# Performance work log

Hardware: AMD Instinct MI355X
Metric: run time of the kernel (lower is better)

Reference implementation:

```python
import jax, jax.numpy as jnp
import numpy as np

N_NODES = 50000
N_EDGES = 800000
D_IN = 128
D_HID = 128
D_OUT = 128
EPS = 0.1  # GINConv eps


def setup_inputs() -> dict:
    key = jax.random.key(0)
    k = jax.random.split(key, 8)
    scale = 1.0 / np.sqrt(D_IN)
    return {
        "x": jax.random.normal(k[0], (N_NODES, D_IN), dtype=jnp.float32),
        "edge_index": jax.random.randint(k[1], (2, N_EDGES), 0, N_NODES, dtype=jnp.int64),
        "edge_weight": jax.random.uniform(k[2], (N_EDGES,), dtype=jnp.float32),
        "W1a": jax.random.normal(k[3], (D_IN, D_HID), dtype=jnp.float32) * scale,
        "W1b": jax.random.normal(k[4], (D_HID, D_HID), dtype=jnpp.float32) if False else jax.random.normal(k[4], (D_HID, D_HID), dtype=jnp.float32) * scale,
        "W2a": jax.random.normal(k[5], (D_HID, D_HID), dtype=jnp.float32) * scale,
        "W2b": jax.random.normal(k[6], (D_HID, D_OUT), dtype=jnp.float32) * scale,
    }


def _gin_conv(h, src, dst, ew, Wa, Wb, n_nodes):
    # edge-weighted neighbor sum: aggr[i] = sum_{(j->i)} w_ji * h[j]
    msg = ew[:, None] * h[src]                       # [E, d]
    aggr = jax.ops.segment_sum(msg, dst, num_segments=n_nodes)  # [N, d]
    z = (1.0 + EPS) * h + aggr                       # GIN update
    # 2-layer bias-free MLP: lin -> relu -> lin
    return jnp.maximum(z @ Wa, 0.0) @ Wb


def reference(x, edge_index, edge_weight, W1a, W1b, W2a, W2b):
    src, dst = edge_index[0], edge_index[1]
    n = x.shape[0]
    h = _gin_conv(x, src, dst, edge_weight, W1a, W1b, n)
    h = jnp.maximum(h, 0.0)  # relu between convs; dropout is identity in eval
    h = _gin_conv(h, src, dst, edge_weight, W2a, W2b, n)
    return h
```

## Files before the change

kernel.cpp:

```cpp
#include <hip/hip_runtime.h>
#include <hip/hip_fp16.h>

#define D 128
#define N_NODES 50000
#define EPSP1 1.1f

#define NPB 256
#define NBUCK 196
#define CAP 5120
#define P1E 2048
#define TS 136

typedef __attribute__((ext_vector_type(8))) short short8;
typedef __attribute__((ext_vector_type(4))) float f32x4;

__device__ __forceinline__ unsigned short f2bf(float f) {
    unsigned u = __float_as_uint(f);
    u += 0x7FFF + ((u >> 16) & 1);
    return (unsigned short)(u >> 16);
}
__device__ __forceinline__ float bf2f(unsigned short h) {
    return __uint_as_float(((unsigned)h) << 16);
}

__global__ __launch_bounds__(256) void pass1_bucket(
    const int* __restrict__ src, const int* __restrict__ dst,
    const float* __restrict__ ew, int* __restrict__ gcnt,
    uint2* __restrict__ gstage, int ne)
{
    __shared__ int bcnt[NBUCK];
    __shared__ int goff[NBUCK];
    int tid = threadIdx.x;
    int bid = blockIdx.x;
    if (tid < NBUCK) bcnt[tid] = 0;
    __syncthreads();
    int e0 = bid * P1E;
    int   rank[8];
    int   buck[8];
    uint2 pay[8];
#pragma unroll
    for (int j = 0; j < 8; ++j) {
        int e = e0 + j * 256 + tid;
        buck[j] = -1;
        if (e < ne) {
            int d_ = dst[e];
            int b  = d_ >> 8;
            int dl = d_ & 255;
            pay[j].x = (unsigned)(src[e] & 0xFFFF) | ((unsigned)dl << 16);
            pay[j].y = (unsigned)__half_as_ushort(__float2half_rn(ew[e]));
            rank[j]  = atomicAdd(&bcnt[b], 1);
            buck[j]  = b;
        }
    }
    __syncthreads();
    if (tid < NBUCK && bcnt[tid] > 0)
        goff[tid] = atomicAdd(&gcnt[tid], bcnt[tid]);
    __syncthreads();
#pragma unroll
    for (int j = 0; j < 8; ++j) {
        if (buck[j] >= 0) {
            int pos = goff[buck[j]] + rank[j];
            if (pos < CAP)
                gstage[(size_t)buck[j] * CAP + pos] = pay[j];
        }
    }
}

__global__ __launch_bounds__(512) void fused_mid(
    const uint2* __restrict__ gstage, const int* __restrict__ gcnt,
    unsigned* __restrict__ epay, int* __restrict__ off,
    const float* __restrict__ x, unsigned short* __restrict__ hb, int n4,
    const float* __restrict__ W1a, const float* __restrict__ W1b,
    const float* __restrict__ W2a, const float* __restrict__ W2b,
    unsigned short* __restrict__ wp)
{
    __shared__ int hist[NPB];
    __shared__ int scn[NPB];
    __shared__ int loc[NPB];
    __shared__ int wtot[8];
    __shared__ int base_s;
    __shared__ unsigned csr[CAP];

    int bid = blockIdx.x;
    int t = threadIdx.x;

    if (bid < NBUCK) {
        int b = bid;
        int cnt = min(gcnt[b], CAP);

        if (t < NPB) hist[t] = 0;
        __syncthreads();

        uint2 ent[CAP / 512];
#pragma unroll
        for (int it = 0; it < CAP / 512; ++it) {
            int i = it * 512 + t;
            if (i < cnt) {
                ent[it] = gstage[(size_t)b * CAP + i];
                atomicAdd(&hist[(ent[it].x >> 16) & 255], 1);
            }
        }
        __syncthreads();

        int w = t >> 6, l = t & 63;
        if (w < 4) {
            int v = hist[w * 64 + l];
#pragma unroll
            for (int dd = 1; dd < 64; dd <<= 1) {
                int u = __shfl_up(v, dd, 64);
                if (l >= dd) v += u;
            }
            scn[w * 64 + l] = v;
            if (l == 63) wtot[w] = v;
        } else if (w == 4) {
            int v = 0;
            for (int i = l; i < NBUCK; i += 64)
                if (i < b) v += min(gcnt[i], CAP);
#pragma unroll
            for (int dd = 32; dd > 0; dd >>= 1) v += __shfl_down(v, dd, 64);
            if (l == 0) base_s = v;
        }
        __syncthreads();

        if (t < NPB) {
            int pre = 0;
#pragma unroll
            for (int j = 0; j < 3; ++j) if (j < w) pre += wtot[j];
            int incl = scn[t] + pre;
            int excl = incl - hist[t];
            int node = (b << 8) + t;
            if (node <= N_NODES) off[node] = base_s + excl;
            loc[t] = excl;
        }
        __syncthreads();

#pragma unroll
        for (int it = 0; it < CAP / 512; ++it) {
            int i = it * 512 + t;
            if (i < cnt) {
                int dl = (ent[it].x >> 16) & 255;
                int p = atomicAdd(&loc[dl], 1);
                csr[p] = (ent[it].x & 0xFFFF) | (ent[it].y << 16);
            }
        }
        __syncthreads();

        for (int i = t; i < cnt; i += 512)
            epay[base_s + i] = csr[i];
    } else if (bid < NBUCK + 782) {
        int base = (bid - NBUCK) * 2048;
#pragma unroll
        for (int it = 0; it < 4; ++it) {
            int i = base + it * 512 + t;
            if (i < n4) {
                float4 v = ((const float4*)x)[i];
                ushort4 o;
                o.x = f2bf(v.x); o.y = f2bf(v.y); o.z = f2bf(v.z); o.w = f2bf(v.w);
                ((ushort4*)hb)[i] = o;
            }
        }
    } else {
        int e2 = (bid - NBUCK - 782) * 512 + t;
        int mat = e2 >> 11;
        int e   = e2 & 2047;
        const float* W = (mat == 0) ? W1a : (mat == 1) ? W1b : (mat == 2) ? W2a : W2b;
        unsigned short* Wp = wp + (size_t)mat * 16384;
        int col = e & 127;
        int kq  = e >> 7;
        short8 v;
#pragma unroll
        for (int j = 0; j < 8; ++j)
            v[j] = (short)f2bf(W[(size_t)(kq * 8 + j) * 128 + col]);
        ((short8*)Wp)[e] = v;
    }
}

__global__ __launch_bounds__(256) void gather_kernel(
    const unsigned short* __restrict__ h, const int* __restrict__ off,
    const unsigned* __restrict__ epay, unsigned short* __restrict__ z, int n_nodes)
{
    int tid = threadIdx.x;
    int node = blockIdx.x * 4 + (tid >> 6);
    if (node >= n_nodes) return;
    int lane = tid & 63;
    int qtr  = lane >> 4;
    int sub  = lane & 15;
    int beg = off[node];
    int end = off[node + 1];
    float acc[8];
#pragma unroll
    for (int c = 0; c < 8; ++c) acc[c] = 0.f;

    int i = beg;
    for (; i + 16 <= end; i += 16) {
        unsigned p0 = epay[i + qtr];
        unsigned p1 = epay[i + 4 + qtr];
        unsigned p2 = epay[i + 8 + qtr];
        unsigned p3 = epay[i + 12 + qtr];
        short8 v0 = ((const short8*)(h + (size_t)(p0 & 0xFFFF) * D))[sub];
        short8 v1 = ((const short8*)(h + (size_t)(p1 & 0xFFFF) * D))[sub];
        short8 v2 = ((const short8*)(h + (size_t)(p2 & 0xFFFF) * D))[sub];
        short8 v3 = ((const short8*)(h + (size_t)(p3 & 0xFFFF) * D))[sub];
        float w0 = __half2float(__ushort_as_half((unsigned short)(p0 >> 16)));
        float w1 = __half2float(__ushort_as_half((unsigned short)(p1 >> 16)));
        float w2 = __half2float(__ushort_as_half((unsigned short)(p2 >> 16)));
        float w3 = __half2float(__ushort_as_half((unsigned short)(p3 >> 16)));
#pragma unroll
        for (int c = 0; c < 8; ++c)
            acc[c] += w0 * bf2f((unsigned short)v0[c]) + w1 * bf2f((unsigned short)v1[c])
                    + w2 * bf2f((unsigned short)v2[c]) + w3 * bf2f((unsigned short)v3[c]);
    }
    for (; i + 8 <= end; i += 8) {
        unsigned p0 = epay[i + qtr];
        unsigned p1 = epay[i + 4 + qtr];
        short8 v0 = ((const short8*)(h + (size_t)(p0 & 0xFFFF) * D))[sub];
        short8 v1 = ((const short8*)(h + (size_t)(p1 & 0xFFFF) * D))[sub];
        float w0 = __half2float(__ushort_as_half((unsigned short)(p0 >> 16)));
        float w1 = __half2float(__ushort_as_half((unsigned short)(p1 >> 16)));
#pragma unroll
        for (int c = 0; c < 8; ++c)
            acc[c] += w0 * bf2f((unsigned short)v0[c]) + w1 * bf2f((unsigned short)v1[c]);
    }
    for (; i + qtr < end; i += 4) {
        unsigned p0 = epay[i + qtr];
        short8 v0 = ((const short8*)(h + (size_t)(p0 & 0xFFFF) * D))[sub];
        float w0 = __half2float(__ushort_as_half((unsigned short)(p0 >> 16)));
#pragma unroll
        for (int c = 0; c < 8; ++c)
            acc[c] += w0 * bf2f((unsigned short)v0[c]);
    }

#pragma unroll
    for (int c = 0; c < 8; ++c) {
        acc[c] += __shfl(acc[c], (lane + 32) & 63, 64);
        acc[c] += __shfl(acc[c], (lane + 16) & 63, 64);
    }

    if (qtr == 0) {
        short8 xv = ((const short8*)(h + (size_t)node * D))[sub];
        short8 o;
#pragma unroll
        for (int c = 0; c < 8; ++c) {
            float v = acc[c] + EPSP1 * bf2f((unsigned short)xv[c]);
            o[c] = (short)f2bf(v);
        }
        ((short8*)(z + (size_t)node * D))[sub] = o;
    }
}

template<int RELU2, int OUT_F32>
__global__ __launch_bounds__(256) void mlp_fused(
    const unsigned short* __restrict__ A,
    const unsigned short* __restrict__ WpA,
    const unsigned short* __restrict__ WpB,
    void* __restrict__ outv, int n)
{
    __shared__ unsigned short t[128 * TS];

    int tid  = threadIdx.x;
    int wave = tid >> 6;
    int lane = tid & 63;
    int quad = lane >> 4;
    int lc   = lane & 15;
    int rbase = blockIdx.x * 128 + wave * 32;
    int rloc  = wave * 32;

    const short8 zero8 = {0, 0, 0, 0, 0, 0, 0, 0};

    short8 a[2][4];
#pragma unroll
    for (int s = 0; s < 2; ++s) {
        int row = rbase + s * 16 + lc;
        const unsigned short* ap = A + (size_t)row * D;
#pragma unroll
        for (int kk = 0; kk < 4; ++kk)
            a[s][kk] = (row < n) ? *(const short8*)(ap + kk * 32 + quad * 8) : zero8;
    }

    f32x4 acc[2][8];
#pragma unroll
    for (int s = 0; s < 2; ++s)
#pragma unroll
        for (int c = 0; c < 8; ++c)
            acc[s][c] = (f32x4){0.f, 0.f, 0.f, 0.f};

#pragma unroll
    for (int cf = 0; cf < 8; ++cf) {
        short8 b[4];
#pragma unroll
        for (int kk = 0; kk < 4; ++kk)
            b[kk] = *(const short8*)(WpA + ((size_t)(kk * 4 + quad) * 128 + cf * 16 + lc) * 8);
#pragma unroll
        for (int kk = 0; kk < 4; ++kk) {
            acc[0][cf] = __builtin_amdgcn_mfma_f32_16x16x32_bf16(a[0][kk], b[kk], acc[0][cf], 0, 0, 0);
            acc[1][cf] = __builtin_amdgcn_mfma_f32_16x16x32_bf16(a[1][kk], b[kk], acc[1][cf], 0, 0, 0);
        }
    }

#pragma unroll
    for (int s = 0; s < 2; ++s)
#pragma unroll
        for (int reg = 0; reg < 4; ++reg) {
            int row = rloc + s * 16 + quad * 4 + reg;
#pragma unroll
            for (int cf = 0; cf < 8; ++cf)
                t[row * TS + cf * 16 + lc] = f2bf(fmaxf(acc[s][cf][reg], 0.f));
        }
    __syncthreads();

#pragma unroll
    for (int s = 0; s < 2; ++s) {
        int row = rloc + s * 16 + lc;
#pragma unroll
        for (int kk = 0; kk < 4; ++kk)
            a[s][kk] = *(const short8*)&t[row * TS + kk * 32 + quad * 8];
    }
#pragma unroll
    for (int s = 0; s < 2; ++s)
#pragma unroll
        for (int c = 0; c < 8; ++c)
            acc[s][c] = (f32x4){0.f, 0.f, 0.f, 0.f};

#pragma unroll
    for (int cf = 0; cf < 8; ++cf) {
        short8 b[4];
#pragma unroll
        for (int kk = 0; kk < 4; ++kk)
            b[kk] = *(const short8*)(WpB + ((size_t)(kk * 4 + quad) * 128 + cf * 16 + lc) * 8);
#pragma unroll
        for (int kk = 0; kk < 4; ++kk) {
            acc[0][cf] = __builtin_amdgcn_mfma_f32_16x16x32_bf16(a[0][kk], b[kk], acc[0][cf], 0, 0, 0);
            acc[1][cf] = __builtin_amdgcn_mfma_f32_16x16x32_bf16(a[1][kk], b[kk], acc[1][cf], 0, 0, 0);
        }
    }

#pragma unroll
    for (int s = 0; s < 2; ++s)
#pragma unroll
        for (int reg = 0; reg < 4; ++reg) {
            int row = rbase + s * 16 + quad * 4 + reg;
            if (row < n) {
#pragma unroll
                for (int cf = 0; cf < 8; ++cf) {
                    float v = acc[s][cf][reg];
                    if (RELU2) v = fmaxf(v, 0.f);
                    int col = cf * 16 + lc;
                    if (OUT_F32)
                        ((float*)outv)[(size_t)row * D + col] = v;
                    else
                        ((unsigned short*)outv)[(size_t)row * D + col] = f2bf(v);
                }
            }
        }
}

extern "C" void kernel_launch(void* const* d_in, const int* in_sizes, int n_in,
                              void* d_out, int out_size, void* d_ws, size_t ws_size,
                              hipStream_t stream) {
    const float* x   = (const float*)d_in[0];
    const int*   ei  = (const int*)d_in[1];
    const float* ew  = (const float*)d_in[2];
    const float* W1a = (const float*)d_in[3];
    const float* W1b = (const float*)d_in[4];
    const float* W2a = (const float*)d_in[5];
    const float* W2b = (const float*)d_in[6];
    float* out = (float*)d_out;

    int n_edges = in_sizes[2];
    const int* src = ei;
    const int* dst = ei + n_edges;

    size_t node_elems = (size_t)N_NODES * D;
    unsigned short* hb = (unsigned short*)d_ws;
    unsigned short* zb = hb + node_elems;
    unsigned short* wp = zb + node_elems;
    unsigned* epay = (unsigned*)(wp + 4 * 16384);
    uint2*  gstage = (uint2*)(epay + n_edges);
    int*    gcnt   = (int*)(gstage + (size_t)NBUCK * CAP);
    int*    off    = gcnt + NBUCK;

    int p1grid = (n_edges + P1E - 1) / P1E;
    int ggrid  = (N_NODES + 127) / 128;
    int agrid  = (N_NODES + 3) / 4;
    int n4     = (int)(node_elems / 4);

    hipMemsetAsync(gcnt, 0, NBUCK * sizeof(int), stream);

    pass1_bucket<<<p1grid, 256, 0, stream>>>(src, dst, ew, gcnt, gstage, n_edges);

    fused_mid<<<NBUCK + 782 + 16, 512, 0, stream>>>(
        gstage, gcnt, epay, off,
        x, hb, n4, W1a, W1b, W2a, W2b, wp);

    unsigned short* wp0 = wp;
    unsigned short* wp1 = wp + 16384;
    unsigned short* wp2 = wp + 2 * 16384;
    unsigned short* wp3 = wp + 3 * 16384;

    gather_kernel<<<agrid, 256, 0, stream>>>(hb, off, epay, zb, N_NODES);
    mlp_fused<1, 0><<<ggrid, 256, 0, stream>>>(zb, wp0, wp1, hb, N_NODES);

    gather_kernel<<<agrid, 256, 0, stream>>>(hb, off, epay, zb, N_NODES);
    mlp_fused<0, 1><<<ggrid, 256, 0, stream>>>(zb, wp2, wp3, out, N_NODES);
}
```

Measured before the change: 202.8 us.

## Fuse neighbor gather with MLP per conv and move conversions into bucketing pass

The gather kernel and the two-layer MLP kernel are merged into one conv kernel. Each wave aggregates 16 nodes into shared memory, then runs both MFMA matmuls on them, so the intermediate z tensor never goes through global memory. Conv 1 now writes its output to zb and conv 2 reads from zb, which avoids overwriting hb while other blocks still gather from it. The x-to-bf16 and weight-packing work moves from the CSR build kernel into the edge-bucketing kernel, and the CSR build kernel keeps only bucket processing. The trade-off is that gathers are serialized per wave over 16 nodes, which can lower memory-level parallelism, and the MLP now runs on 16-row tiles per wave, so weights are reused less.

New measurement: 277.7 us. 36.9% more time.

```diff
diff --git a/kernel.cpp b/kernel.cpp
--- a/kernel.cpp
+++ b/kernel.cpp
@@ -23,56 +23,87 @@
     return __uint_as_float(((unsigned)h) << 16);
 }
 
-__global__ __launch_bounds__(256) void pass1_bucket(
+__global__ __launch_bounds__(256) void pass1_all(
     const int* __restrict__ src, const int* __restrict__ dst,
     const float* __restrict__ ew, int* __restrict__ gcnt,
-    uint2* __restrict__ gstage, int ne)
+    uint2* __restrict__ gstage, int ne, int nb1,
+    const float* __restrict__ x, unsigned short* __restrict__ hb,
+    int n4, int ncvt,
+    const float* __restrict__ W1a, const float* __restrict__ W1b,
+    const float* __restrict__ W2a, const float* __restrict__ W2b,
+    unsigned short* __restrict__ wp)
 {
     __shared__ int bcnt[NBUCK];
     __shared__ int goff[NBUCK];
     int tid = threadIdx.x;
     int bid = blockIdx.x;
-    if (tid < NBUCK) bcnt[tid] = 0;
-    __syncthreads();
-    int e0 = bid * P1E;
-    int   rank[8];
-    int   buck[8];
-    uint2 pay[8];
-#pragma unroll
-    for (int j = 0; j < 8; ++j) {
-        int e = e0 + j * 256 + tid;
-        buck[j] = -1;
-        if (e < ne) {
-            int d_ = dst[e];
-            int b  = d_ >> 8;
-            int dl = d_ & 255;
-            pay[j].x = (unsigned)(src[e] & 0xFFFF) | ((unsigned)dl << 16);
-            pay[j].y = (unsigned)__half_as_ushort(__float2half_rn(ew[e]));
-            rank[j]  = atomicAdd(&bcnt[b], 1);
-            buck[j]  = b;
-        }
-    }
-    __syncthreads();
-    if (tid < NBUCK && bcnt[tid] > 0)
-        goff[tid] = atomicAdd(&gcnt[tid], bcnt[tid]);
-    __syncthreads();
-#pragma unroll
-    for (int j = 0; j < 8; ++j) {
-        if (buck[j] >= 0) {
-            int pos = goff[buck[j]] + rank[j];
-            if (pos < CAP)
-                gstage[(size_t)buck[j] * CAP + pos] = pay[j];
-        }
-    }
-}
-
-__global__ __launch_bounds__(512) void fused_mid(
+
+    if (bid < nb1) {
+        if (tid < NBUCK) bcnt[tid] = 0;
+        __syncthreads();
+        int e0 = bid * P1E;
+        int   rank[8];
+        int   buck[8];
+        uint2 pay[8];
+#pragma unroll
+        for (int j = 0; j < 8; ++j) {
+            int e = e0 + j * 256 + tid;
+            buck[j] = -1;
+            if (e < ne) {
+                int d_ = dst[e];
+                int b  = d_ >> 8;
+                int dl = d_ & 255;
+                pay[j].x = (unsigned)(src[e] & 0xFFFF) | ((unsigned)dl << 16);
+                pay[j].y = (unsigned)__half_as_ushort(__float2half_rn(ew[e]));
+                rank[j]  = atomicAdd(&bcnt[b], 1);
+                buck[j]  = b;
+            }
+        }
+        __syncthreads();
+        if (tid < NBUCK && bcnt[tid] > 0)
+            goff[tid] = atomicAdd(&gcnt[tid], bcnt[tid]);
+        __syncthreads();
+#pragma unroll
+        for (int j = 0; j < 8; ++j) {
+            if (buck[j] >= 0) {
+                int pos = goff[buck[j]] + rank[j];
+                if (pos < CAP)
+                    gstage[(size_t)buck[j] * CAP + pos] = pay[j];
+            }
+        }
+    } else if (bid < nb1 + ncvt) {
+        int base = (bid - nb1) * 2048;
+#pragma unroll
+        for (int it = 0; it < 8; ++it) {
+            int i = base + it * 256 + tid;
+            if (i < n4) {
+                float4 v = ((const float4*)x)[i];
+                ushort4 o;
+                o.x = f2bf(v.x); o.y = f2bf(v.y); o.z = f2bf(v.z); o.w = f2bf(v.w);
+                ((ushort4*)hb)[i] = o;
+            }
+        }
+    } else {
+        int e2 = (bid - nb1 - ncvt) * 256 + tid;
+        if (e2 < 8192) {
+            int mat = e2 >> 11;
+            int e   = e2 & 2047;
+            const float* W = (mat == 0) ? W1a : (mat == 1) ? W1b : (mat == 2) ? W2a : W2b;
+            unsigned short* Wp = wp + (size_t)mat * 16384;
+            int col = e & 127;
+            int kq  = e >> 7;
+            short8 v;
+#pragma unroll
+            for (int j = 0; j < 8; ++j)
+                v[j] = (short)f2bf(W[(size_t)(kq * 8 + j) * 128 + col]);
+            ((short8*)Wp)[e] = v;
+        }
+    }
+}
+
+__global__ __launch_bounds__(512) void csr_build(
     const uint2* __restrict__ gstage, const int* __restrict__ gcnt,
-    unsigned* __restrict__ epay, int* __restrict__ off,
-    const float* __restrict__ x, unsigned short* __restrict__ hb, int n4,
-    const float* __restrict__ W1a, const float* __restrict__ W1b,
-    const float* __restrict__ W2a, const float* __restrict__ W2b,
-    unsigned short* __restrict__ wp)
+    unsigned* __restrict__ epay, int* __restrict__ off)
 {
     __shared__ int hist[NPB];
     __shared__ int scn[NPB];
@@ -81,277 +112,226 @@
     __shared__ int base_s;
     __shared__ unsigned csr[CAP];
 
-    int bid = blockIdx.x;
+    int b = blockIdx.x;
     int t = threadIdx.x;
-
-    if (bid < NBUCK) {
-        int b = bid;
-        int cnt = min(gcnt[b], CAP);
-
-        if (t < NPB) hist[t] = 0;
-        __syncthreads();
-
-        uint2 ent[CAP / 512];
-#pragma unroll
-        for (int it = 0; it < CAP / 512; ++it) {
-            int i = it * 512 + t;
-            if (i < cnt) {
-                ent[it] = gstage[(size_t)b * CAP + i];
-                atomicAdd(&hist[(ent[it].x >> 16) & 255], 1);
-            }
-        }
-        __syncthreads();
-
-        int w = t >> 6, l = t & 63;
-        if (w < 4) {
-            int v = hist[w * 64 + l];
-#pragma unroll
-            for (int dd = 1; dd < 64; dd <<= 1) {
-                int u = __shfl_up(v, dd, 64);
-                if (l >= dd) v += u;
-            }
-            scn[w * 64 + l] = v;
-            if (l == 63) wtot[w] = v;
-        } else if (w == 4) {
-            int v = 0;
-            for (int i = l; i < NBUCK; i += 64)
-                if (i < b) v += min(gcnt[i], CAP);
-#pragma unroll
-            for (int dd = 32; dd > 0; dd >>= 1) v += __shfl_down(v, dd, 64);
-            if (l == 0) base_s = v;
-        }
-        __syncthreads();
-
-        if (t < NPB) {
-            int pre = 0;
-#pragma unroll
-            for (int j = 0; j < 3; ++j) if (j < w) pre += wtot[j];
-            int incl = scn[t] + pre;
-            int excl = incl - hist[t];
-            int node = (b << 8) + t;
-            if (node <= N_NODES) off[node] = base_s + excl;
-            loc[t] = excl;
-        }
-        __syncthreads();
-
-#pragma unroll
-        for (int it = 0; it < CAP / 512; ++it) {
-            int i = it * 512 + t;
-            if (i < cnt) {
-                int dl = (ent[it].x >> 16) & 255;
-                int p = atomicAdd(&loc[dl], 1);
-                csr[p] = (ent[it].x & 0xFFFF) | (ent[it].y << 16);
-            }
-        }
-        __syncthreads();
-
-        for (int i = t; i < cnt; i += 512)
-            epay[base_s + i] = csr[i];
-    } else if (bid < NBUCK + 782) {
-        int base = (bid - NBUCK) * 2048;
-#pragma unroll
-        for (int it = 0; it < 4; ++it) {
-            int i = base + it * 512 + t;
-            if (i < n4) {
-                float4 v = ((const float4*)x)[i];
-                ushort4 o;
-                o.x = f2bf(v.x); o.y = f2bf(v.y); o.z = f2bf(v.z); o.w = f2bf(v.w);
-                ((ushort4*)hb)[i] = o;
-            }
-        }
-    } else {
-        int e2 = (bid - NBUCK - 782) * 512 + t;
-        int mat = e2 >> 11;
-        int e   = e2 & 2047;
-        const float* W = (mat == 0) ? W1a : (mat == 1) ? W1b : (mat == 2) ? W2a : W2b;
-        unsigned short* Wp = wp + (size_t)mat * 16384;
-        int col = e & 127;
-        int kq  = e >> 7;
-        short8 v;
-#pragma unroll
-        for (int j = 0; j < 8; ++j)
-            v[j] = (short)f2bf(W[(size_t)(kq * 8 + j) * 128 + col]);
-        ((short8*)Wp)[e] = v;
-    }
-}
-
-__global__ __launch_bounds__(256) void gather_kernel(
+    int cnt = min(gcnt[b], CAP);
+
+    if (t < NPB) hist[t] = 0;
+    __syncthreads();
+
+    uint2 ent[CAP / 512];
+#pragma unroll
+    for (int it = 0; it < CAP / 512; ++it) {
+        int i = it * 512 + t;
+        if (i < cnt) {
+            ent[it] = gstage[(size_t)b * CAP + i];
+            atomicAdd(&hist[(ent[it].x >> 16) & 255], 1);
+        }
+    }
+    __syncthreads();
+
+    int w = t >> 6, l = t & 63;
+    if (w < 4) {
+        int v = hist[w * 64 + l];
+#pragma unroll
+        for (int dd = 1; dd < 64; dd <<= 1) {
+            int u = __shfl_up(v, dd, 64);
+            if (l >= dd) v += u;
+        }
+        scn[w * 64 + l] = v;
+        if (l == 63) wtot[w] = v;
+    } else if (w == 4) {
+        int v = 0;
+        for (int i = l; i < NBUCK; i += 64)
+            if (i < b) v += min(gcnt[i], CAP);
+#pragma unroll
+        for (int dd = 32; dd > 0; dd >>= 1) v += __shfl_down(v, dd, 64);
+        if (l == 0) base_s = v;
+    }
+    __syncthreads();
+
+    if (t < NPB) {
+        int pre = 0;
+#pragma unroll
+        for (int j = 0; j < 3; ++j) if (j < w) pre += wtot[j];
+        int incl = scn[t] + pre;
+        int excl = incl - hist[t];
+        int node = (b << 8) + t;
+        if (node <= N_NODES) off[node] = base_s + excl;
+        loc[t] = excl;
+    }
+    __syncthreads();
+
+#pragma unroll
+    for (int it = 0; it < CAP / 512; ++it) {
+        int i = it * 512 + t;
+        if (i < cnt) {
+            int dl = (ent[it].x >> 16) & 255;
+            int p = atomicAdd(&loc[dl], 1);
+            csr[p] = (ent[it].x & 0xFFFF) | (ent[it].y << 16);
+        }
+    }
+    __syncthreads();
+
+    for (int i = t; i < cnt; i += 512)
+        epay[base_s + i] = csr[i];
+}
+
+template<int RELU2, int OUT_F32>
+__global__ __launch_bounds__(256) void conv_fused(
     const unsigned short* __restrict__ h, const int* __restrict__ off,
-    const unsigned* __restrict__ epay, unsigned short* __restrict__ z, int n_nodes)
-{
-    int tid = threadIdx.x;
-    int node = blockIdx.x * 4 + (tid >> 6);
-    if (node >= n_nodes) return;
-    int lane = tid & 63;
-    int qtr  = lane >> 4;
-    int sub  = lane & 15;
-    int beg = off[node];
-    int end = off[node + 1];
-    float acc[8];
-#pragma unroll
-    for (int c = 0; c < 8; ++c) acc[c] = 0.f;
-
-    int i = beg;
-    for (; i + 16 <= end; i += 16) {
-        unsigned p0 = epay[i + qtr];
-        unsigned p1 = epay[i + 4 + qtr];
-        unsigned p2 = epay[i + 8 + qtr];
-        unsigned p3 = epay[i + 12 + qtr];
-        short8 v0 = ((const short8*)(h + (size_t)(p0 & 0xFFFF) * D))[sub];
-        short8 v1 = ((const short8*)(h + (size_t)(p1 & 0xFFFF) * D))[sub];
-        short8 v2 = ((const short8*)(h + (size_t)(p2 & 0xFFFF) * D))[sub];
-        short8 v3 = ((const short8*)(h + (size_t)(p3 & 0xFFFF) * D))[sub];
-        float w0 = __half2float(__ushort_as_half((unsigned short)(p0 >> 16)));
-        float w1 = __half2float(__ushort_as_half((unsigned short)(p1 >> 16)));
-        float w2 = __half2float(__ushort_as_half((unsigned short)(p2 >> 16)));
-        float w3 = __half2float(__ushort_as_half((unsigned short)(p3 >> 16)));
-#pragma unroll
-        for (int c = 0; c < 8; ++c)
-            acc[c] += w0 * bf2f((unsigned short)v0[c]) + w1 * bf2f((unsigned short)v1[c])
-                    + w2 * bf2f((unsigned short)v2[c]) + w3 * bf2f((unsigned short)v3[c]);
-    }
-    for (; i + 8 <= end; i += 8) {
-        unsigned p0 = epay[i + qtr];
-        unsigned p1 = epay[i + 4 + qtr];
-        short8 v0 = ((const short8*)(h + (size_t)(p0 & 0xFFFF) * D))[sub];
-        short8 v1 = ((const short8*)(h + (size_t)(p1 & 0xFFFF) * D))[sub];
-        float w0 = __half2float(__ushort_as_half((unsigned short)(p0 >> 16)));
-        float w1 = __half2float(__ushort_as_half((unsigned short)(p1 >> 16)));
-#pragma unroll
-        for (int c = 0; c < 8; ++c)
-            acc[c] += w0 * bf2f((unsigned short)v0[c]) + w1 * bf2f((unsigned short)v1[c]);
-    }
-    for (; i + qtr < end; i += 4) {
-        unsigned p0 = epay[i + qtr];
-        short8 v0 = ((const short8*)(h + (size_t)(p0 & 0xFFFF) * D))[sub];
-        float w0 = __half2float(__ushort_as_half((unsigned short)(p0 >> 16)));
-#pragma unroll
-        for (int c = 0; c < 8; ++c)
-            acc[c] += w0 * bf2f((unsigned short)v0[c]);
-    }
-
-#pragma unroll
-    for (int c = 0; c < 8; ++c) {
-        acc[c] += __shfl(acc[c], (lane + 32) & 63, 64);
-        acc[c] += __shfl(acc[c], (lane + 16) & 63, 64);
-    }
-
-    if (qtr == 0) {
-        short8 xv = ((const short8*)(h + (size_t)node * D))[sub];
-        short8 o;
-#pragma unroll
-        for (int c = 0; c < 8; ++c) {
-            float v = acc[c] + EPSP1 * bf2f((unsigned short)xv[c]);
-            o[c] = (short)f2bf(v);
-        }
-        ((short8*)(z + (size_t)node * D))[sub] = o;
-    }
-}
-
-template<int RELU2, int OUT_F32>
-__global__ __launch_bounds__(256) void mlp_fused(
-    const unsigned short* __restrict__ A,
+    const unsigned* __restrict__ epay,
     const unsigned short* __restrict__ WpA,
     const unsigned short* __restrict__ WpB,
     void* __restrict__ outv, int n)
 {
-    __shared__ unsigned short t[128 * TS];
+    __shared__ unsigned short t[64 * TS];
 
     int tid  = threadIdx.x;
     int wave = tid >> 6;
     int lane = tid & 63;
-    int quad = lane >> 4;
-    int lc   = lane & 15;
-    int rbase = blockIdx.x * 128 + wave * 32;
-    int rloc  = wave * 32;
+    int qtr  = lane >> 4;
+    int sub  = lane & 15;
+    int rloc  = wave * 16;
+    int rbase = blockIdx.x * 64 + rloc;
 
     const short8 zero8 = {0, 0, 0, 0, 0, 0, 0, 0};
 
-    short8 a[2][4];
-#pragma unroll
-    for (int s = 0; s < 2; ++s) {
-        int row = rbase + s * 16 + lc;
-        const unsigned short* ap = A + (size_t)row * D;
-#pragma unroll
-        for (int kk = 0; kk < 4; ++kk)
-            a[s][kk] = (row < n) ? *(const short8*)(ap + kk * 32 + quad * 8) : zero8;
-    }
-
-    f32x4 acc[2][8];
-#pragma unroll
-    for (int s = 0; s < 2; ++s)
-#pragma unroll
-        for (int c = 0; c < 8; ++c)
-            acc[s][c] = (f32x4){0.f, 0.f, 0.f, 0.f};
+    for (int nd = 0; nd < 16; ++nd) {
+        int node = rbase + nd;
+        float acc[8];
+#pragma unroll
+        for (int c = 0; c < 8; ++c) acc[c] = 0.f;
+
+        if (node < n) {
+            int beg = off[node];
+            int end = off[node + 1];
+            int i = beg;
+            for (; i + 16 <= end; i += 16) {
+                unsigned p0 = epay[i + qtr];
+                unsigned p1 = epay[i + 4 + qtr];
+                unsigned p2 = epay[i + 8 + qtr];
+                unsigned p3 = epay[i + 12 + qtr];
+                short8 v0 = ((const short8*)(h + (size_t)(p0 & 0xFFFF) * D))[sub];
+                short8 v1 = ((const short8*)(h + (size_t)(p1 & 0xFFFF) * D))[sub];
+                short8 v2 = ((const short8*)(h + (size_t)(p2 & 0xFFFF) * D))[sub];
+                short8 v3 = ((const short8*)(h + (size_t)(p3 & 0xFFFF) * D))[sub];
+                float w0 = __half2float(__ushort_as_half((unsigned short)(p0 >> 16)));
+                float w1 = __half2float(__ushort_as_half((unsigned short)(p1 >> 16)));
+                float w2 = __half2float(__ushort_as_half((unsigned short)(p2 >> 16)));
+                float w3 = __half2float(__ushort_as_half((unsigned short)(p3 >> 16)));
+#pragma unroll
+                for (int c = 0; c < 8; ++c)
+                    acc[c] += w0 * bf2f((unsigned short)v0[c]) + w1 * bf2f((unsigned short)v1[c])
+                            + w2 * bf2f((unsigned short)v2[c]) + w3 * bf2f((unsigned short)v3[c]);
+            }
+            for (; i + 8 <= end; i += 8) {
+                unsigned p0 = epay[i + qtr];
+                unsigned p1 = epay[i + 4 + qtr];
+                short8 v0 = ((const short8*)(h + (size_t)(p0 & 0xFFFF) * D))[sub];
+                short8 v1 = ((const short8*)(h + (size_t)(p1 & 0xFFFF) * D))[sub];
+                float w0 = __half2float(__ushort_as_half((unsigned short)(p0 >> 16)));
+                float w1 = __half2float(__ushort_as_half((unsigned short)(p1 >> 16)));
+#pragma unroll
+                for (int c = 0; c < 8; ++c)
+                    acc[c] += w0 * bf2f((unsigned short)v0[c]) + w1 * bf2f((unsigned short)v1[c]);
+            }
+            for (; i + qtr < end; i += 4) {
+                unsigned p0 = epay[i + qtr];
+                short8 v0 = ((const short8*)(h + (size_t)(p0 & 0xFFFF) * D))[sub];
+                float w0 = __half2float(__ushort_as_half((unsigned short)(p0 >> 16)));
+#pragma unroll
+                for (int c = 0; c < 8; ++c)
+                    acc[c] += w0 * bf2f((unsigned short)v0[c]);
+            }
+        }
+
+#pragma unroll
+        for (int c = 0; c < 8; ++c) {
+            acc[c] += __shfl(acc[c], (lane + 32) & 63, 64);
+            acc[c] += __shfl(acc[c], (lane + 16) & 63, 64);
+        }
+
+        if (qtr == 0) {
+            short8 o;
+            if (node < n) {
+                short8 xv = ((const short8*)(h + (size_t)node * D))[sub];
+#pragma unroll
+                for (int c = 0; c < 8; ++c)
+                    o[c] = (short)f2bf(acc[c] + EPSP1 * bf2f((unsigned short)xv[c]));
+            } else {
+                o = zero8;
+            }
+            *(short8*)&t[(rloc + nd) * TS + sub * 8] = o;
+        }
+    }
+
+    short8 a[4];
+    {
+        int row = rloc + sub;
+#pragma unroll
+        for (int kk = 0; kk < 4; ++kk)
+            a[kk] = *(const short8*)&t[row * TS + kk * 32 + qtr * 8];
+    }
+    f32x4 acc2[8];
+#pragma unroll
+    for (int c = 0; c < 8; ++c) acc2[c] = (f32x4){0.f, 0.f, 0.f, 0.f};
 
 #pragma unroll
     for (int cf = 0; cf < 8; ++cf) {
         short8 b[4];
 #pragma unroll
         for (int kk = 0; kk < 4; ++kk)
-            b[kk] = *(const short8*)(WpA + ((size_t)(kk * 4 + quad) * 128 + cf * 16 + lc) * 8);
-#pragma unroll
-        for (int kk = 0; kk < 4; ++kk) {
-            acc[0][cf] = __builtin_amdgcn_mfma_f32_16x16x32_bf16(a[0][kk], b[kk], acc[0][cf], 0, 0, 0);
-            acc[1][cf] = __builtin_amdgcn_mfma_f32_16x16x32_bf16(a[1][kk], b[kk], acc[1][cf], 0, 0, 0);
-        }
-    }
-
-#pragma unroll
-    for (int s = 0; s < 2; ++s)
-#pragma unroll
-        for (int reg = 0; reg < 4; ++reg) {
-            int row = rloc + s * 16 + quad * 4 + reg;
-#pragma unroll
-            for (int cf = 0; cf < 8; ++cf)
-                t[row * TS + cf * 16 + lc] = f2bf(fmaxf(acc[s][cf][reg], 0.f));
-        }
-    __syncthreads();
-
-#pragma unroll
-    for (int s = 0; s < 2; ++s) {
-        int row = rloc + s * 16 + lc;
-#pragma unroll
-        for (int kk = 0; kk < 4; ++kk)
-            a[s][kk] = *(const short8*)&t[row * TS + kk * 32 + quad * 8];
-    }
-#pragma unroll
-    for (int s = 0; s < 2; ++s)
-#pragma unroll
-        for (int c = 0; c < 8; ++c)
-            acc[s][c] = (f32x4){0.f, 0.f, 0.f, 0.f};
+            b[kk] = *(const short8*)(WpA + ((size_t)(kk * 4 + qtr) * 128 + cf * 16 + sub) * 8);
+#pragma unroll
+        for (int kk = 0; kk < 4; ++kk)
+            acc2[cf] = __builtin_amdgcn_mfma_f32_16x16x32_bf16(a[kk], b[kk], acc2[cf], 0, 0, 0);
+    }
+
+#pragma unroll
+    for (int reg = 0; reg < 4; ++reg) {
+        int row = rloc + qtr * 4 + reg;
+#pragma unroll
+        for (int cf = 0; cf < 8; ++cf)
+            t[row * TS + cf * 16 + sub] = f2bf(fmaxf(acc2[cf][reg], 0.f));
+    }
+
+    {
+        int row = rloc + sub;
+#pragma unroll
+        for (int kk = 0; kk < 4; ++kk)
+            a[kk] = *(const short8*)&t[row * TS + kk * 32 + qtr * 8];
+    }
+#pragma unroll
+    for (int c = 0; c < 8; ++c) acc2[c] = (f32x4){0.f, 0.f, 0.f, 0.f};
 
 #pragma unroll
     for (int cf = 0; cf < 8; ++cf) {
         short8 b[4];
 #pragma unroll
         for (int kk = 0; kk < 4; ++kk)
-            b[kk] = *(const short8*)(WpB + ((size_t)(kk * 4 + quad) * 128 + cf * 16 + lc) * 8);
-#pragma unroll
-        for (int kk = 0; kk < 4; ++kk) {
-            acc[0][cf] = __builtin_amdgcn_mfma_f32_16x16x32_bf16(a[0][kk], b[kk], acc[0][cf], 0, 0, 0);
-            acc[1][cf] = __builtin_amdgcn_mfma_f32_16x16x32_bf16(a[1][kk], b[kk], acc[1][cf], 0, 0, 0);
-        }
-    }
-
-#pragma unroll
-    for (int s = 0; s < 2; ++s)
-#pragma unroll
-        for (int reg = 0; reg < 4; ++reg) {
-            int row = rbase + s * 16 + quad * 4 + reg;
-            if (row < n) {
-#pragma unroll
-                for (int cf = 0; cf < 8; ++cf) {
-                    float v = acc[s][cf][reg];
-                    if (RELU2) v = fmaxf(v, 0.f);
-                    int col = cf * 16 + lc;
-                    if (OUT_F32)
-                        ((float*)outv)[(size_t)row * D + col] = v;
-                    else
-                        ((unsigned short*)outv)[(size_t)row * D + col] = f2bf(v);
-                }
-            }
-        }
+            b[kk] = *(const short8*)(WpB + ((size_t)(kk * 4 + qtr) * 128 + cf * 16 + sub) * 8);
+#pragma unroll
+        for (int kk = 0; kk < 4; ++kk)
+            acc2[cf] = __builtin_amdgcn_mfma_f32_16x16x32_bf16(a[kk], b[kk], acc2[cf], 0, 0, 0);
+    }
+
+#pragma unroll
+    for (int reg = 0; reg < 4; ++reg) {
+        int row = rbase + qtr * 4 + reg;
+        if (row < n) {
+#pragma unroll
+            for (int cf = 0; cf < 8; ++cf) {
+                float v = acc2[cf][reg];
+                if (RELU2) v = fmaxf(v, 0.f);
+                int col = cf * 16 + sub;
+                if (OUT_F32)
+                    ((float*)outv)[(size_t)row * D + col] = v;
+                else
+                    ((unsigned short*)outv)[(size_t)row * D + col] = f2bf(v);
+            }
+        }
+    }
 }
 
 extern "C" void kernel_launch(void* const* d_in, const int* in_sizes, int n_in,
@@ -379,27 +359,26 @@
     int*    gcnt   = (int*)(gstage + (size_t)NBUCK * CAP);
     int*    off    = gcnt + NBUCK;
 
-    int p1grid = (n_edges + P1E - 1) / P1E;
-    int ggrid  = (N_NODES + 127) / 128;
-    int agrid  = (N_NODES + 3) / 4;
-    int n4     = (int)(node_elems / 4);
+    int nb1   = (n_edges + P1E - 1) / P1E;
+    int n4    = (int)(node_elems / 4);
+    int ncvt  = (n4 + 2047) / 2048;
+    int npack = 32;
+    int cgrid = (N_NODES + 63) / 64;
 
     hipMemsetAsync(gcnt, 0, NBUCK * sizeof(int), stream);
 
-    pass1_bucket<<<p1grid, 256, 0, stream>>>(src, dst, ew, gcnt, gstage, n_edges);
-
-    fused_mid<<<NBUCK + 782 + 16, 512, 0, stream>>>(
-        gstage, gcnt, epay, off,
-        x, hb, n4, W1a, W1b, W2a, W2b, wp);
+    pass1_all<<<nb1 + ncvt + npack, 256, 0, stream>>>(
+        src, dst, ew, gcnt, gstage, n_edges, nb1,
+        x, hb, n4, ncvt, W1a, W1b, W2a, W2b, wp);
+
+    csr_build<<<NBUCK, 512, 0, stream>>>(gstage, gcnt, epay, off);
 
     unsigned short* wp0 = wp;
     unsigned short* wp1 = wp + 16384;
     unsigned short* wp2 = wp + 2 * 16384;
     unsigned short* wp3 = wp + 3 * 16384;
 
-    gather_kernel<<<agrid, 256, 0, stream>>>(hb, off, epay, zb, N_NODES);
-    mlp_fused<1, 0><<<ggrid, 256, 0, stream>>>(zb, wp0, wp1, hb, N_NODES);
-
-    gather_kernel<<<agrid, 256, 0, stream>>>(hb, off, epay, zb, N_NODES);
-    mlp_fused<0, 1><<<ggrid, 256, 0, stream>>>(zb, wp2, wp3, out, N_NODES);
-}
+    conv_fused<1, 0><<<cgrid, 256, 0, stream>>>(hb, off, epay, wp0, wp1, zb, N_NODES);
+
+    conv_fused<0, 1><<<cgrid, 256, 0, stream>>>(zb, off, epay, wp2, wp3, out, N_NODES);
+}
```
